# Kernel tuning notes

Measured on AMD Instinct MI355X. Metric: run time of the kernel, lower is better.

The kernel has to match this reference:

```python
import jax, jax.numpy as jnp
import numpy as np

B, S, D, H = 2, 2048, 2048, 16
DH = D // H            # 128 head dim
QP = D // 2            # 1024 compressed q dim
KVP = (2 * D) // 3     # 1365 compressed kv dim
RD = DH // 2           # 64 rope dim
ND = DH // 2           # 64 nope dim
FF = 4 * D
THETA = 10000.0


def _ln(x, w, b, eps=1e-5):
    m = jnp.mean(x, -1, keepdims=True)
    v = jnp.mean((x - m) ** 2, -1, keepdims=True)
    return (x - m) * jax.lax.rsqrt(v + eps) * w + b


def _rotate_half(x):
    x1, x2 = jnp.split(x, 2, axis=-1)
    return jnp.concatenate([-x2, x1], axis=-1)


def setup_inputs() -> dict:
    key = jax.random.key(0)
    ks = jax.random.split(key, 9)
    rn = lambda k, shp, s: (s * jax.random.normal(k, shp)).astype(jnp.float32)
    return {
        'x': jax.random.normal(ks[0], (B, S, D), jnp.float32),
        'attn_norm_w': jnp.ones((D,), jnp.float32), 'attn_norm_b': jnp.zeros((D,), jnp.float32),
        'W_dq': rn(ks[1], (D, QP), 0.01),
        'q_ln_w': jnp.ones((QP,), jnp.float32), 'q_ln_b': jnp.zeros((QP,), jnp.float32),
        'W_uq': rn(ks[2], (QP, D), 0.01),
        'W_dkv': rn(ks[3], (D, KVP + RD), 0.01),
        'kv_ln_w': jnp.ones((KVP,), jnp.float32), 'kv_ln_b': jnp.zeros((KVP,), jnp.float32),
        'W_ukv': rn(ks[4], (KVP, D + H * ND), 0.01),
        'W_o': rn(ks[5], (D, D), 0.01),
        'ff_norm_w': jnp.ones((D,), jnp.float32), 'ff_norm_b': jnp.zeros((D,), jnp.float32),
        'W1': rn(ks[6], (D, FF), 0.02), 'b1': jnp.zeros((FF,), jnp.float32),
        'W2': rn(ks[7], (FF, D), 0.02), 'b2': jnp.zeros((D,), jnp.float32),
    }


def reference(x, attn_norm_w, attn_norm_b, W_dq, q_ln_w, q_ln_b, W_uq, W_dkv,
              kv_ln_w, kv_ln_b, W_ukv, W_o, ff_norm_w, ff_norm_b, W1, b1, W2, b2):
    # ---- pre-LN attention ----
    h = _ln(x, attn_norm_w, attn_norm_b)
    # Q path: down-proj, LN, up-proj
    cq = _ln(h @ W_dq, q_ln_w, q_ln_b)                      # [B,S,QP]
    Q = (cq @ W_uq).reshape(B, S, H, DH).transpose(0, 2, 1, 3)  # [B,H,S,DH]
    Qn, Qr = Q[..., :ND], Q[..., ND:]
    # RoPE tables: emb [S, DH/2]; take first RD/2 freqs, tile -> [1,1,S,RD]
    pos = jnp.arange(S, dtype=jnp.float32)
    freqs = 1.0 / (THETA ** (jnp.arange(0, DH, 2, dtype=jnp.float32) / DH))
    emb = pos[:, None] * freqs[None, :]
    cos = jnp.tile(jnp.cos(emb)[:, :RD // 2], (1, 2))[None, None]
    sin = jnp.tile(jnp.sin(emb)[:, :RD // 2], (1, 2))[None, None]
    Qr = Qr * cos + _rotate_half(Qr) * sin
    # KV path: joint down-proj, split latent / shared rope key
    ckv = h @ W_dkv                                          # [B,S,KVP+RD]
    kv_lora, k_rope = ckv[..., :KVP], ckv[..., KVP:]
    kv_lora = _ln(kv_lora, kv_ln_w, kv_ln_b)
    KV = (kv_lora @ W_ukv).reshape(B, S, H, DH + ND).transpose(0, 2, 1, 3)
    K, V = KV[..., :ND], KV[..., ND:]                        # K [B,H,S,ND], V [B,H,S,DH]
    Kr = k_rope[:, None]                                     # [B,1,S,RD] shared across heads
    Kr = Kr * cos + _rotate_half(Kr) * sin
    Kr = jnp.broadcast_to(Kr, (B, H, S, RD))
    q = jnp.concatenate([Qn, Qr], -1)                        # [B,H,S,DH]
    k = jnp.concatenate([K, Kr], -1)                         # [B,H,S,DH]
    scores = jnp.einsum('bhqd,bhkd->bhqk', q, k) / jnp.sqrt(jnp.float32(DH))
    mask = jnp.tril(jnp.ones((S, S), bool))
    scores = jnp.where(mask, scores, jnp.finfo(scores.dtype).min)
    attn = jax.nn.softmax(scores, axis=-1)
    o = jnp.einsum('bhqk,bhkd->bhqd', attn, V).transpose(0, 2, 1, 3).reshape(B, S, D)
    o = o @ W_o.T
    x = x + o  # dropout is identity at eval
    # ---- pre-LN MLP ----
    r = x
    h = _ln(x, ff_norm_w, ff_norm_b)
    h = jax.nn.gelu(h @ W1 + b1, approximate=False) @ W2 + b2
    return r + h, ckv
```

## Files before the change

### kernel.cpp

```cpp
#include <hip/hip_runtime.h>
#include <hip/hip_bf16.h>
#include <math.h>

#define B_ 2
#define S_ 2048
#define D_ 2048
#define H_ 16
#define DH_ 128
#define QP_ 1024
#define KVP_ 1365
#define RD_ 64
#define ND_ 64
#define FF_ 8192
#define T_ (B_*S_)
#define CKW_ (KVP_+RD_)
#define KVW_ 3072
#define KVP_PAD 1408
#define CKW_PAD 1536

typedef __attribute__((ext_vector_type(8))) short short8;
typedef __attribute__((ext_vector_type(4))) short sh4;
typedef __attribute__((ext_vector_type(4))) float floatx4;

__device__ __forceinline__ void gload_lds16(const __hip_bfloat16* g, __hip_bfloat16* l) {
    __builtin_amdgcn_global_load_lds((const __attribute__((address_space(1))) void*)g,
                                     (__attribute__((address_space(3))) void*)l, 16, 0, 0);
}
__device__ __forceinline__ short f2bs(float f) {
    __hip_bfloat16 h = __float2bfloat16(f);
    return *reinterpret_cast<short*>(&h);
}
__device__ __forceinline__ int sw(int row, int g) { return row * 64 + ((g ^ (row & 7)) << 3); }

__device__ __forceinline__ float fast_gelu(float v) {
    float x = v * 0.70710678118654752f;
    float ax = fabsf(x);
    float t = __builtin_amdgcn_rcpf(1.f + 0.3275911f * ax);
    float y = t * (0.254829592f + t * (-0.284496736f + t * (1.421413741f + t * (-1.453152027f + t * 1.061405429f))));
    float e = __expf(-ax * ax);
    float erfv = 1.f - y * e;
    erfv = copysignf(erfv, x);
    return 0.5f * v * (1.f + erfv);
}

__global__ __launch_bounds__(256) void ln_bf16(const float* __restrict__ in, int in_stride,
                                               const float* __restrict__ w, const float* __restrict__ bb,
                                               __hip_bfloat16* __restrict__ out, int out_stride, int N)
{
    int row = blockIdx.x;
    const float* ip = in + (size_t)row * in_stride;
    __hip_bfloat16* op = out + (size_t)row * out_stride;
    int tid = threadIdx.x;
    __shared__ float s1[256], s2[256];
    float sum = 0.f, sq = 0.f;
    bool vec = (((in_stride | N | out_stride) & 3) == 0);
    if (vec) {
        const float4* ip4 = (const float4*)ip;
        int n4 = N >> 2;
        for (int i = tid; i < n4; i += 256) {
            float4 v = ip4[i];
            sum += v.x + v.y + v.z + v.w;
            sq  += v.x * v.x + v.y * v.y + v.z * v.z + v.w * v.w;
        }
        s1[tid] = sum; s2[tid] = sq; __syncthreads();
        for (int s = 128; s > 0; s >>= 1) {
            if (tid < s) { s1[tid] += s1[tid + s]; s2[tid] += s2[tid + s]; }
            __syncthreads();
        }
        float mean = s1[0] / N;
        float var  = s2[0] / N - mean * mean;
        float rstd = rsqrtf(var + 1e-5f);
        const float4* w4 = (const float4*)w;
        const float4* b4 = (const float4*)bb;
        for (int i = tid; i < n4; i += 256) {
            float4 v = ip4[i], wv = w4[i], bv = b4[i];
            sh4 o;
            o[0] = f2bs((v.x - mean) * rstd * wv.x + bv.x);
            o[1] = f2bs((v.y - mean) * rstd * wv.y + bv.y);
            o[2] = f2bs((v.z - mean) * rstd * wv.z + bv.z);
            o[3] = f2bs((v.w - mean) * rstd * wv.w + bv.w);
            *(sh4*)&op[i * 4] = o;
        }
    } else {
        for (int i = tid; i < N; i += 256) { float v = ip[i]; sum += v; sq += v * v; }
        s1[tid] = sum; s2[tid] = sq; __syncthreads();
        for (int s = 128; s > 0; s >>= 1) {
            if (tid < s) { s1[tid] += s1[tid + s]; s2[tid] += s2[tid + s]; }
            __syncthreads();
        }
        float mean = s1[0] / N;
        float var  = s2[0] / N - mean * mean;
        float rstd = rsqrtf(var + 1e-5f);
        for (int i = tid; i < N; i += 256) {
            float v = ip[i];
            op[i] = __float2bfloat16((v - mean) * rstd * w[i] + bb[i]);
        }
    }
    for (int i = N + tid; i < out_stride; i += 256) op[i] = __float2bfloat16(0.f);
}

__global__ __launch_bounds__(256) void transpose_cvt(const float* __restrict__ W, __hip_bfloat16* __restrict__ Wt,
                                                     int K, int N, int Kp)
{
    __shared__ float t[32][33];
    int k0 = blockIdx.x * 32, n0 = blockIdx.y * 32;
    int tx = threadIdx.x & 31, ty = threadIdx.x >> 5;
    for (int r = ty; r < 32; r += 8) {
        int k = k0 + r, n = n0 + tx;
        t[r][tx] = (k < K && n < N) ? W[(size_t)k * N + n] : 0.f;
    }
    __syncthreads();
    for (int r = ty; r < 32; r += 8) {
        int n = n0 + r, k = k0 + tx;
        Wt[(size_t)n * Kp + k] = __float2bfloat16(t[tx][r]);
    }
}

__global__ __launch_bounds__(256) void cvt_bf16(const float* __restrict__ in, __hip_bfloat16* __restrict__ out, int n)
{
    int i = blockIdx.x * 256 + threadIdx.x;
    if (i < n) out[i] = __float2bfloat16(in[i]);
}

template<int EPI, typename CT>
__global__ __launch_bounds__(256) void gemm_bf16(const __hip_bfloat16* __restrict__ A,
                                                 const __hip_bfloat16* __restrict__ Bt,
                                                 CT* __restrict__ C, int M, int N, int Kp, int ldc,
                                                 const float* __restrict__ bias,
                                                 const float* __restrict__ resid)
{
    __shared__ __hip_bfloat16 As[128 * 64];
    __shared__ __hip_bfloat16 Bs[128 * 64];
    int tid = threadIdx.x;
    int gx = gridDim.x;
    int nwg = gx * gridDim.y;
    int o = blockIdx.y * gx + blockIdx.x;
    int sId = ((nwg & 7) == 0) ? ((o & 7) * (nwg >> 3) + (o >> 3)) : o;
    int bm = (sId / gx) * 128;
    int bn = (sId % gx) * 128;
    int wid = tid >> 6, lane = tid & 63;
    int wm = (wid >> 1) * 64, wn = (wid & 1) * 64;
    int lrow = lane & 15;
    int quad = lane >> 4;

    floatx4 acc[4][4];
    #pragma unroll
    for (int i = 0; i < 4; ++i)
        #pragma unroll
        for (int j = 0; j < 4; ++j)
            acc[i][j] = (floatx4){0.f, 0.f, 0.f, 0.f};

    for (int k0 = 0; k0 < Kp; k0 += 64) {
        #pragma unroll
        for (int it = 0; it < 4; ++it) {
            int chunk = it * 256 + tid;
            int row = chunk >> 3, g = chunk & 7;
            int col = (g ^ (row & 7)) << 3;
            gload_lds16(A + (size_t)(bm + row) * Kp + k0 + col, &As[chunk * 8]);
        }
        #pragma unroll
        for (int it = 0; it < 4; ++it) {
            int chunk = it * 256 + tid;
            int row = chunk >> 3, g = chunk & 7;
            int col = (g ^ (row & 7)) << 3;
            gload_lds16(Bt + (size_t)(bn + row) * Kp + k0 + col, &Bs[chunk * 8]);
        }
        __syncthreads();
        #pragma unroll
        for (int kk = 0; kk < 2; ++kk) {
            short8 a[4], b[4];
            #pragma unroll
            for (int i = 0; i < 4; ++i)
                a[i] = *(const short8*)&As[sw(wm + i * 16 + lrow, kk * 4 + quad)];
            #pragma unroll
            for (int j = 0; j < 4; ++j)
                b[j] = *(const short8*)&Bs[sw(wn + j * 16 + lrow, kk * 4 + quad)];
            #pragma unroll
            for (int i = 0; i < 4; ++i)
                #pragma unroll
                for (int j = 0; j < 4; ++j)
                    acc[i][j] = __builtin_amdgcn_mfma_f32_16x16x32_bf16(a[i], b[j], acc[i][j], 0, 0, 0);
        }
        __syncthreads();
    }

    int cq4 = quad * 4;
    #pragma unroll
    for (int i = 0; i < 4; ++i) {
        #pragma unroll
        for (int j = 0; j < 4; ++j) {
            int col = bn + wn + j * 16 + lrow;
            if (col >= N) continue;
            #pragma unroll
            for (int r = 0; r < 4; ++r) {
                int rowg = bm + wm + i * 16 + cq4 + r;
                float v = acc[i][j][r];
                size_t idx = (size_t)rowg * ldc + col;
                if (EPI == 1) v += resid[idx];
                if (EPI == 2) { v += bias[col]; v = fast_gelu(v); }
                if (EPI == 3) { v += bias[col]; v += ((const float*)C)[idx]; }
                C[idx] = (CT)v;
            }
        }
    }
}

#define BAR8() __builtin_amdgcn_s_barrier()
#define SCB8() __builtin_amdgcn_sched_barrier(0)
#define GATE8(nw) asm volatile("s_waitcnt vmcnt(" #nw ")" ::: "memory")

template<int EPI, typename CT>
__global__ __launch_bounds__(512, 1) void gemm_8ph(const __hip_bfloat16* __restrict__ A,
                                                   const __hip_bfloat16* __restrict__ Bt,
                                                   CT* __restrict__ C, int M, int N, int Kp, int ldc,
                                                   const float* __restrict__ bias,
                                                   const float* __restrict__ resid)
{
    __shared__ __hip_bfloat16 As[2][16384];
    __shared__ __hip_bfloat16 Bs[2][16384];

    int tid = threadIdx.x;
    int wid = tid >> 6, lane = tid & 63;
    int lrow = lane & 15, quad = lane >> 4;
    int awm = (wid >> 2) * 128;
    int bwn = (wid & 3) * 64;

    int gx = gridDim.x;
    int nwg = gx * gridDim.y;
    int o = blockIdx.y * gx + blockIdx.x;
    int q8 = nwg >> 3, r8 = nwg & 7;
    int xcd = o & 7, oi = o >> 3;
    int s = (xcd < r8 ? xcd * (q8 + 1) : r8 * (q8 + 1) + (xcd - r8) * q8) + oi;
    int bm = (s / gx) * 256, bn = (s % gx) * 256;

    const __hip_bfloat16* Abm = A  + (size_t)bm * Kp;
    const __hip_bfloat16* Bbn = Bt + (size_t)bn * Kp;

    int drow = tid >> 3;
    int csw  = ((tid & 7) ^ (drow & 7)) << 3;
    int ldst = tid * 8;

#define STAGE8(srcbase, k0v, dst) do { \
    gload_lds16((srcbase) + (size_t)drow * Kp + (k0v) + csw, (dst) + ldst); \
    gload_lds16((srcbase) + (size_t)(drow + 64) * Kp + (k0v) + csw, (dst) + 4096 + ldst); \
  } while (0)

    int abase = awm + lrow;
    int bbase = bwn + lrow;
    int k0off = ((quad       ^ (lrow & 7)) << 3);
    int k1off = (((4 + quad) ^ (lrow & 7)) << 3);

    short8 af[8][2], bfr[4][2];
    floatx4 acc[8][4];
    #pragma unroll
    for (int m = 0; m < 8; ++m)
        #pragma unroll
        for (int n = 0; n < 4; ++n)
            acc[m][n] = (floatx4){0.f, 0.f, 0.f, 0.f};

#define READ_A8(bufp, mh) do { \
    _Pragma("unroll") \
    for (int m = 0; m < 4; ++m) { \
      const __hip_bfloat16* p_ = (bufp) + (abase + ((mh)*4 + m) * 16) * 64; \
      af[(mh)*4 + m][0] = *(const short8*)(p_ + k0off); \
      af[(mh)*4 + m][1] = *(const short8*)(p_ + k1off); \
    } } while (0)

#define READ_B8(bufp, nh) do { \
    _Pragma("unroll") \
    for (int n = 0; n < 2; ++n) { \
      const __hip_bfloat16* p_ = (bufp) + (bbase + ((nh)*2 + n) * 16) * 64; \
      bfr[(nh)*2 + n][0] = *(const short8*)(p_ + k0off); \
      bfr[(nh)*2 + n][1] = *(const short8*)(p_ + k1off); \
    } } while (0)

#define QMFMA8(mh, nh) do { \
    __builtin_amdgcn_s_setprio(1); \
    _Pragma("unroll") \
    for (int kk = 0; kk < 2; ++kk) \
      _Pragma("unroll") \
      for (int m = 0; m < 4; ++m) \
        _Pragma("unroll") \
        for (int n = 0; n < 2; ++n) \
          acc[(mh)*4 + m][(nh)*2 + n] = __builtin_amdgcn_mfma_f32_16x16x32_bf16( \
              af[(mh)*4 + m][kk], bfr[(nh)*2 + n][kk], acc[(mh)*4 + m][(nh)*2 + n], 0, 0, 0); \
    __builtin_amdgcn_s_setprio(0); \
  } while (0)

    STAGE8(Abm,                   0,  &As[0][0]);
    STAGE8(Abm + (size_t)128*Kp,  0,  &As[0][8192]);
    STAGE8(Bbn,                   0,  &Bs[0][0]);
    STAGE8(Bbn + (size_t)128*Kp,  0,  &Bs[0][8192]);
    STAGE8(Abm,                   64, &As[1][0]);
    STAGE8(Abm + (size_t)128*Kp,  64, &As[1][8192]);
    GATE8(4); SCB8(); BAR8();

    int NT = Kp >> 6;
    #pragma unroll 1
    for (int t = 0; t < NT; t += 2) {
        int kn = (t + 1) << 6;
        int k2 = ((t + 2 < NT) ? t + 2 : NT - 1) << 6;
        int k3 = ((t + 3 < NT) ? t + 3 : NT - 1) << 6;

        STAGE8(Bbn, kn, &Bs[1][0]);
        READ_A8(&As[0][0], 0); READ_B8(&Bs[0][0], 0);
        SCB8(); BAR8();
        QMFMA8(0, 0);
        SCB8(); BAR8();
        STAGE8(Bbn + (size_t)128*Kp, kn, &Bs[1][8192]);
        READ_B8(&Bs[0][0], 1);
        SCB8(); BAR8();
        QMFMA8(0, 1);
        SCB8(); BAR8();
        READ_A8(&As[0][0], 1);
        SCB8(); BAR8();
        QMFMA8(1, 1);
        SCB8(); BAR8();
        STAGE8(Abm, k2, &As[0][0]);
        STAGE8(Abm + (size_t)128*Kp, k2, &As[0][8192]);
        SCB8(); BAR8();
        QMFMA8(1, 0);
        GATE8(4); SCB8(); BAR8();
        STAGE8(Bbn, k2, &Bs[0][0]);
        READ_A8(&As[1][0], 0); READ_B8(&Bs[1][0], 0);
        SCB8(); BAR8();
        QMFMA8(0, 0);
        SCB8(); BAR8();
        STAGE8(Bbn + (size_t)128*Kp, k2, &Bs[0][8192]);
        READ_B8(&Bs[1][0], 1);
        SCB8(); BAR8();
        QMFMA8(0, 1);
        SCB8(); BAR8();
        READ_A8(&As[1][0], 1);
        SCB8(); BAR8();
        QMFMA8(1, 1);
        SCB8(); BAR8();
        STAGE8(Abm, k3, &As[1][0]);
        STAGE8(Abm + (size_t)128*Kp, k3, &As[1][8192]);
        SCB8(); BAR8();
        QMFMA8(1, 0);
        GATE8(4); SCB8(); BAR8();
    }
    asm volatile("s_waitcnt vmcnt(0)" ::: "memory");

    int cq4 = quad * 4;
    #pragma unroll
    for (int m = 0; m < 8; ++m) {
        int rowg = bm + awm + m * 16 + cq4;
        #pragma unroll
        for (int n = 0; n < 4; ++n) {
            int col = bn + bwn + n * 16 + lrow;
            #pragma unroll
            for (int r = 0; r < 4; ++r) {
                float v = acc[m][n][r];
                size_t idx = (size_t)(rowg + r) * ldc + col;
                if (EPI == 1) v += resid[idx];
                if (EPI == 2) { v += bias[col]; v = fast_gelu(v); }
                if (EPI == 3) { v += bias[col]; v += ((const float*)C)[idx]; }
                C[idx] = (CT)v;
            }
        }
    }
#undef STAGE8
#undef READ_A8
#undef READ_B8
#undef QMFMA8
}

__global__ __launch_bounds__(256) void rope_q_kernel(float* __restrict__ Q)
{
    int idx = blockIdx.x * 256 + threadIdx.x;
    int i = idx & 31;
    int h = (idx >> 5) & (H_ - 1);
    int t = idx >> 9;
    float f = expf(-(float)i * (9.210340371976184f / 64.0f));
    float ang = (float)(t & (S_ - 1)) * f;
    float sv, cv; sincosf(ang, &sv, &cv);
    float* p = Q + (size_t)t * D_ + h * DH_ + ND_;
    float u = p[i], v = p[i + 32];
    p[i]      = u * cv - v * sv;
    p[i + 32] = v * cv + u * sv;
}

__global__ __launch_bounds__(256) void rope_kr_bf(const float* __restrict__ ckv, __hip_bfloat16* __restrict__ kr)
{
    int idx = blockIdx.x * 256 + threadIdx.x;
    int i = idx & 31;
    int t = idx >> 5;
    float f = expf(-(float)i * (9.210340371976184f / 64.0f));
    float ang = (float)(t & (S_ - 1)) * f;
    float sv, cv; sincosf(ang, &sv, &cv);
    const float* src = ckv + (size_t)t * CKW_ + KVP_;
    float u = src[i], v = src[i + 32];
    kr[(size_t)t * RD_ + i]      = __float2bfloat16(u * cv - v * sv);
    kr[(size_t)t * RD_ + i + 32] = __float2bfloat16(v * cv + u * sv);
}

__global__ __launch_bounds__(256) void vt_pack(const __hip_bfloat16* __restrict__ kvu,
                                               __hip_bfloat16* __restrict__ Vt)
{
    int bh = blockIdx.y; int b = bh >> 4, h = bh & 15;
    int v = threadIdx.x & 127;
    int tg = blockIdx.x * 2 + (threadIdx.x >> 7);
    int t0 = tg * 8;
    short8 o;
    #pragma unroll
    for (int j = 0; j < 8; ++j) {
        __hip_bfloat16 e = kvu[(size_t)(b * S_ + t0 + j) * KVW_ + h * 192 + 64 + v];
        o[j] = *reinterpret_cast<short*>(&e);
    }
    *(short8*)&Vt[((size_t)bh * 128 + v) * S_ + t0] = o;
}

__global__ __launch_bounds__(256) void attn_mfma(const float* __restrict__ Q,
                                                 const __hip_bfloat16* __restrict__ KVU,
                                                 const __hip_bfloat16* __restrict__ KR,
                                                 const __hip_bfloat16* __restrict__ VT,
                                                 __hip_bfloat16* __restrict__ O)
{
    __shared__ __hip_bfloat16 Kls[64 * 64];
    __shared__ __hip_bfloat16 Krls[64 * 64];
    __shared__ __hip_bfloat16 Vls[128 * 64];
    __shared__ __hip_bfloat16 Pls[4 * 32 * 64];

    int tid = threadIdx.x, wid = tid >> 6, lane = tid & 63;
    int lrow = lane & 15, quad = lane >> 4;
    int kq8 = quad * 8;
    int o = blockIdx.y * 16 + blockIdx.x;
    int sId = (o & 7) * 64 + (o >> 3);
    int qtile = 15 - (sId & 15);
    int bh = sId >> 4;
    int b = bh >> 4, h = bh & 15;
    int q0 = qtile * 128, wq = wid * 32;

    const float scale = 0.08838834764831845f;

    short8 bq[2][2], bqr[2][2];
    #pragma unroll
    for (int n = 0; n < 2; ++n) {
        const float* qrow = Q + (size_t)(b * S_ + q0 + wq + n * 16 + lrow) * D_ + h * DH_;
        #pragma unroll
        for (int s = 0; s < 2; ++s) {
            int base = s * 32 + kq8;
            #pragma unroll
            for (int j = 0; j < 8; ++j) {
                bq[n][s][j]  = f2bs(qrow[base + j] * scale);
                bqr[n][s][j] = f2bs(qrow[64 + base + j] * scale);
            }
        }
    }

    float mstate[2] = {-INFINITY, -INFINITY};
    float lstate[2] = {0.f, 0.f};
    floatx4 acco[8][2];
    #pragma unroll
    for (int vt = 0; vt < 8; ++vt)
        #pragma unroll
        for (int n = 0; n < 2; ++n)
            acco[vt][n] = (floatx4){0.f, 0.f, 0.f, 0.f};

    int nk = qtile * 2 + 2;
    int qmax_w = q0 + wq + 31;

    for (int kt = 0; kt < nk; ++kt) {
        int k0 = kt * 64;
        #pragma unroll
        for (int it = 0; it < 2; ++it) {
            int c = it * 256 + tid;
            int row = c >> 3, g = c & 7;
            int col = ((g ^ (row & 7)) << 3);
            gload_lds16(KVU + (size_t)(b * S_ + k0 + row) * KVW_ + h * 192 + col, &Kls[c * 8]);
            gload_lds16(KR + (size_t)(b * S_ + k0 + row) * RD_ + col, &Krls[c * 8]);
        }
        #pragma unroll
        for (int it = 0; it < 4; ++it) {
            int c = it * 256 + tid;
            int row = c >> 3, g = c & 7;
            int col = ((g ^ (row & 7)) << 3);
            gload_lds16(VT + ((size_t)bh * 128 + row) * S_ + k0 + col, &Vls[c * 8]);
        }
        __syncthreads();

        if (k0 <= qmax_w) {
            floatx4 sacc[4][2];
            #pragma unroll
            for (int m = 0; m < 4; ++m)
                #pragma unroll
                for (int n = 0; n < 2; ++n)
                    sacc[m][n] = (floatx4){0.f, 0.f, 0.f, 0.f};
            #pragma unroll
            for (int m = 0; m < 4; ++m) {
                short8 ak[2], akr[2];
                #pragma unroll
                for (int s = 0; s < 2; ++s) {
                    ak[s]  = *(const short8*)&Kls[sw(m * 16 + lrow, s * 4 + quad)];
                    akr[s] = *(const short8*)&Krls[sw(m * 16 + lrow, s * 4 + quad)];
                }
                #pragma unroll
                for (int n = 0; n < 2; ++n)
                    #pragma unroll
                    for (int s = 0; s < 2; ++s) {
                        sacc[m][n] = __builtin_amdgcn_mfma_f32_16x16x32_bf16(ak[s],  bq[n][s],  sacc[m][n], 0, 0, 0);
                        sacc[m][n] = __builtin_amdgcn_mfma_f32_16x16x32_bf16(akr[s], bqr[n][s], sacc[m][n], 0, 0, 0);
                    }
            }
            #pragma unroll
            for (int n = 0; n < 2; ++n) {
                int qg = q0 + wq + n * 16 + lrow;
                float tmax = -INFINITY;
                #pragma unroll
                for (int m = 0; m < 4; ++m)
                    #pragma unroll
                    for (int r = 0; r < 4; ++r) {
                        int kg = k0 + m * 16 + quad * 4 + r;
                        if (kg > qg) sacc[m][n][r] = -1e30f;
                        tmax = fmaxf(tmax, sacc[m][n][r]);
                    }
                tmax = fmaxf(tmax, __shfl_xor(tmax, 16));
                tmax = fmaxf(tmax, __shfl_xor(tmax, 32));
                float mnew = fmaxf(mstate[n], tmax);
                float alpha = __expf(mstate[n] - mnew);
                mstate[n] = mnew;
                float ps = 0.f;
                #pragma unroll
                for (int m = 0; m < 4; ++m) {
                    sh4 pk;
                    #pragma unroll
                    for (int r = 0; r < 4; ++r) {
                        float p = __expf(sacc[m][n][r] - mnew);
                        ps += p;
                        pk[r] = f2bs(p);
                    }
                    int qloc = n * 16 + lrow;
                    int off = wid * 2048 + qloc * 64 + (((m * 2 + (quad >> 1)) ^ (lrow & 7)) << 3) + ((quad & 1) << 2);
                    *(sh4*)&Pls[off] = pk;
                }
                ps += __shfl_xor(ps, 16);
                ps += __shfl_xor(ps, 32);
                lstate[n] = lstate[n] * alpha + ps;
                #pragma unroll
                for (int vt = 0; vt < 8; ++vt)
                    #pragma unroll
                    for (int r = 0; r < 4; ++r)
                        acco[vt][n][r] *= alpha;
            }
            short8 bp[2][2];
            #pragma unroll
            for (int n = 0; n < 2; ++n)
                #pragma unroll
                for (int s = 0; s < 2; ++s)
                    bp[n][s] = *(const short8*)&Pls[wid * 2048 + sw(n * 16 + lrow, s * 4 + quad)];
            #pragma unroll
            for (int vt = 0; vt < 8; ++vt) {
                short8 av[2];
                #pragma unroll
                for (int s = 0; s < 2; ++s)
                    av[s] = *(const short8*)&Vls[sw(vt * 16 + lrow, s * 4 + quad)];
                #pragma unroll
                for (int n = 0; n < 2; ++n)
                    #pragma unroll
                    for (int s = 0; s < 2; ++s)
                        acco[vt][n] = __builtin_amdgcn_mfma_f32_16x16x32_bf16(av[s], bp[n][s], acco[vt][n], 0, 0, 0);
            }
        }
        __syncthreads();
    }

    #pragma unroll
    for (int n = 0; n < 2; ++n) {
        float inv = 1.0f / lstate[n];
        int tok = b * S_ + q0 + wq + n * 16 + lrow;
        #pragma unroll
        for (int vt = 0; vt < 8; ++vt) {
            sh4 o4;
            #pragma unroll
            for (int r = 0; r < 4; ++r) o4[r] = f2bs(acco[vt][n][r] * inv);
            *(sh4*)&O[(size_t)tok * D_ + h * DH_ + vt * 16 + quad * 4] = o4;
        }
    }
}

extern "C" void kernel_launch(void* const* d_in, const int* in_sizes, int n_in,
                              void* d_out, int out_size, void* d_ws, size_t ws_size,
                              hipStream_t stream)
{
    const float* x     = (const float*)d_in[0];
    const float* anw   = (const float*)d_in[1];
    const float* anb   = (const float*)d_in[2];
    const float* W_dq  = (const float*)d_in[3];
    const float* qlw   = (const float*)d_in[4];
    const float* qlb   = (const float*)d_in[5];
    const float* W_uq  = (const float*)d_in[6];
    const float* W_dkv = (const float*)d_in[7];
    const float* kvlw  = (const float*)d_in[8];
    const float* kvlb  = (const float*)d_in[9];
    const float* W_ukv = (const float*)d_in[10];
    const float* W_o   = (const float*)d_in[11];
    const float* fnw   = (const float*)d_in[12];
    const float* fnb   = (const float*)d_in[13];
    const float* W1    = (const float*)d_in[14];
    const float* b1    = (const float*)d_in[15];
    const float* W2    = (const float*)d_in[16];
    const float* b2    = (const float*)d_in[17];

    float* out0 = (float*)d_out;
    float* ckv  = out0 + (size_t)T_ * D_;

    float* ws = (float*)d_ws;
    float* Q  = ws;
    float* cq = Q + (size_t)T_ * D_;
    __hip_bfloat16* kvu_bf = (__hip_bfloat16*)(cq + (size_t)T_ * QP_);
    __hip_bfloat16* kr_bf  = kvu_bf + (size_t)T_ * KVW_;
    __hip_bfloat16* Vt     = kr_bf + (size_t)T_ * RD_;
    __hip_bfloat16* h_bf   = Vt + (size_t)T_ * D_;
    __hip_bfloat16* cq_bf  = h_bf + (size_t)T_ * D_;
    __hip_bfloat16* kvl_bf = cq_bf + (size_t)T_ * QP_;
    __hip_bfloat16* o_bf   = kvl_bf + (size_t)T_ * KVP_PAD;
    __hip_bfloat16* wdq_t  = o_bf + (size_t)T_ * D_;
    __hip_bfloat16* wuq_t  = wdq_t + (size_t)QP_ * D_;
    __hip_bfloat16* wdkv_t = wuq_t + (size_t)D_ * QP_;
    __hip_bfloat16* wukv_t = wdkv_t + (size_t)CKW_PAD * D_;
    __hip_bfloat16* wo_b   = wukv_t + (size_t)KVW_ * KVP_PAD;
    __hip_bfloat16* w1_t   = wo_b + (size_t)D_ * D_;
    __hip_bfloat16* w2_t   = w1_t + (size_t)FF_ * D_;
    __hip_bfloat16* ff1_bf = (__hip_bfloat16*)ws;

    dim3 blk(256);
    dim3 blk8(512);

    { dim3 g(D_ / 32, QP_ / 32);       transpose_cvt<<<g, blk, 0, stream>>>(W_dq,  wdq_t,  D_, QP_, D_); }
    { dim3 g(QP_ / 32, D_ / 32);       transpose_cvt<<<g, blk, 0, stream>>>(W_uq,  wuq_t,  QP_, D_, QP_); }
    { dim3 g(D_ / 32, CKW_PAD / 32);   transpose_cvt<<<g, blk, 0, stream>>>(W_dkv, wdkv_t, D_, CKW_, D_); }
    { dim3 g(KVP_PAD / 32, KVW_ / 32); transpose_cvt<<<g, blk, 0, stream>>>(W_ukv, wukv_t, KVP_, KVW_, KVP_PAD); }
    { int n = D_ * D_;                 cvt_bf16<<<(n + 255) / 256, blk, 0, stream>>>(W_o, wo_b, n); }
    { dim3 g(D_ / 32, FF_ / 32);       transpose_cvt<<<g, blk, 0, stream>>>(W1, w1_t, D_, FF_, D_); }
    { dim3 g(FF_ / 32, D_ / 32);       transpose_cvt<<<g, blk, 0, stream>>>(W2, w2_t, FF_, D_, FF_); }

    ln_bf16<<<T_, blk, 0, stream>>>(x, D_, anw, anb, h_bf, D_, D_);
    { dim3 g(QP_ / 128, T_ / 128);
      gemm_bf16<0, float><<<g, blk, 0, stream>>>(h_bf, wdq_t, cq, T_, QP_, D_, QP_, nullptr, nullptr); }
    ln_bf16<<<T_, blk, 0, stream>>>(cq, QP_, qlw, qlb, cq_bf, QP_, QP_);
    { dim3 g(D_ / 128, T_ / 128);
      gemm_bf16<0, float><<<g, blk, 0, stream>>>(cq_bf, wuq_t, Q, T_, D_, QP_, D_, nullptr, nullptr); }
    rope_q_kernel<<<(T_ * H_ * 32) / 256, blk, 0, stream>>>(Q);
    { dim3 g(CKW_PAD / 128, T_ / 128);
      gemm_bf16<0, float><<<g, blk, 0, stream>>>(h_bf, wdkv_t, ckv, T_, CKW_, D_, CKW_, nullptr, nullptr); }
    ln_bf16<<<T_, blk, 0, stream>>>(ckv, CKW_, kvlw, kvlb, kvl_bf, KVP_PAD, KVP_);
    { dim3 g(KVW_ / 256, T_ / 256);
      gemm_8ph<0, __hip_bfloat16><<<g, blk8, 0, stream>>>(kvl_bf, wukv_t, kvu_bf, T_, KVW_, KVP_PAD, KVW_, nullptr, nullptr); }
    rope_kr_bf<<<(T_ * 32) / 256, blk, 0, stream>>>(ckv, kr_bf);
    { dim3 g(S_ / 16, B_ * H_);
      vt_pack<<<g, blk, 0, stream>>>(kvu_bf, Vt); }
    { dim3 g(16, B_ * H_);
      attn_mfma<<<g, blk, 0, stream>>>(Q, kvu_bf, kr_bf, Vt, o_bf); }
    { dim3 g(D_ / 128, T_ / 128);
      gemm_bf16<1, float><<<g, blk, 0, stream>>>(o_bf, wo_b, out0, T_, D_, D_, D_, nullptr, x); }
    ln_bf16<<<T_, blk, 0, stream>>>(out0, D_, fnw, fnb, h_bf, D_, D_);
    { dim3 g(FF_ / 256, T_ / 256);
      gemm_8ph<2, __hip_bfloat16><<<g, blk8, 0, stream>>>(h_bf, w1_t, ff1_bf, T_, FF_, D_, FF_, b1, nullptr); }
    { dim3 g(D_ / 128, T_ / 128);
      gemm_bf16<3, float><<<g, blk, 0, stream>>>(ff1_bf, w2_t, out0, T_, D_, FF_, D_, b2, nullptr); }
}
```

Before: 1.070 ms.

## Add 256x128-tile 8-wave pipelined GEMM for N=2048 projections

```diff
diff --git a/kernel.cpp b/kernel.cpp
--- a/kernel.cpp
+++ b/kernel.cpp
@@ -307,34 +307,41 @@
         SCB8(); BAR8();
         QMFMA8(0, 0);
         SCB8(); BAR8();
+
         STAGE8(Bbn + (size_t)128*Kp, kn, &Bs[1][8192]);
         READ_B8(&Bs[0][0], 1);
         SCB8(); BAR8();
         QMFMA8(0, 1);
         SCB8(); BAR8();
+
         READ_A8(&As[0][0], 1);
         SCB8(); BAR8();
         QMFMA8(1, 1);
         SCB8(); BAR8();
+
         STAGE8(Abm, k2, &As[0][0]);
         STAGE8(Abm + (size_t)128*Kp, k2, &As[0][8192]);
         SCB8(); BAR8();
         QMFMA8(1, 0);
         GATE8(4); SCB8(); BAR8();
+
         STAGE8(Bbn, k2, &Bs[0][0]);
         READ_A8(&As[1][0], 0); READ_B8(&Bs[1][0], 0);
         SCB8(); BAR8();
         QMFMA8(0, 0);
         SCB8(); BAR8();
+
         STAGE8(Bbn + (size_t)128*Kp, k2, &Bs[0][8192]);
         READ_B8(&Bs[1][0], 1);
         SCB8(); BAR8();
         QMFMA8(0, 1);
         SCB8(); BAR8();
+
         READ_A8(&As[1][0], 1);
         SCB8(); BAR8();
         QMFMA8(1, 1);
         SCB8(); BAR8();
+
         STAGE8(Abm, k3, &As[1][0]);
         STAGE8(Abm + (size_t)128*Kp, k3, &As[1][8192]);
         SCB8(); BAR8();
@@ -365,6 +372,163 @@
 #undef READ_A8
 #undef READ_B8
 #undef QMFMA8
+}
+
+template<int EPI, typename CT>
+__global__ __launch_bounds__(512, 1) void gemm_8ph_n128(const __hip_bfloat16* __restrict__ A,
+                                                        const __hip_bfloat16* __restrict__ Bt,
+                                                        CT* __restrict__ C, int M, int N, int Kp, int ldc,
+                                                        const float* __restrict__ bias,
+                                                        const float* __restrict__ resid)
+{
+    __shared__ __hip_bfloat16 As[2][16384];
+    __shared__ __hip_bfloat16 Bs[2][8192];
+
+    int tid = threadIdx.x;
+    int wid = tid >> 6, lane = tid & 63;
+    int lrow = lane & 15, quad = lane >> 4;
+    int awm = (wid >> 2) * 128;
+    int bwn = (wid & 3) * 32;
+
+    int gx = gridDim.x;
+    int nwg = gx * gridDim.y;
+    int o = blockIdx.y * gx + blockIdx.x;
+    int q8 = nwg >> 3, r8 = nwg & 7;
+    int xcd = o & 7, oi = o >> 3;
+    int s = (xcd < r8 ? xcd * (q8 + 1) : r8 * (q8 + 1) + (xcd - r8) * q8) + oi;
+    int bm = (s / gx) * 256, bn = (s % gx) * 128;
+
+    const __hip_bfloat16* Abm = A  + (size_t)bm * Kp;
+    const __hip_bfloat16* Bbn = Bt + (size_t)bn * Kp;
+
+    int drow = tid >> 3;
+    int csw  = ((tid & 7) ^ (drow & 7)) << 3;
+    int ldst = tid * 8;
+
+#define STAGE_A(k0v, dst) do { \
+    gload_lds16(Abm + (size_t)drow * Kp + (k0v) + csw,         (dst) + ldst); \
+    gload_lds16(Abm + (size_t)(drow + 64) * Kp + (k0v) + csw,  (dst) + 4096 + ldst); \
+    gload_lds16(Abm + (size_t)(drow + 128) * Kp + (k0v) + csw, (dst) + 8192 + ldst); \
+    gload_lds16(Abm + (size_t)(drow + 192) * Kp + (k0v) + csw, (dst) + 12288 + ldst); \
+  } while (0)
+#define STAGE_B(k0v, dst) do { \
+    gload_lds16(Bbn + (size_t)drow * Kp + (k0v) + csw,        (dst) + ldst); \
+    gload_lds16(Bbn + (size_t)(drow + 64) * Kp + (k0v) + csw, (dst) + 4096 + ldst); \
+  } while (0)
+
+    int abase = awm + lrow;
+    int bbase = bwn + lrow;
+    int k0off = ((quad       ^ (lrow & 7)) << 3);
+    int k1off = (((4 + quad) ^ (lrow & 7)) << 3);
+
+    short8 af[8][2], bfr[2][2];
+    floatx4 acc[8][2];
+    #pragma unroll
+    for (int m = 0; m < 8; ++m)
+        #pragma unroll
+        for (int n = 0; n < 2; ++n)
+            acc[m][n] = (floatx4){0.f, 0.f, 0.f, 0.f};
+
+#define READ_A(bufp, mh) do { \
+    _Pragma("unroll") \
+    for (int m = 0; m < 4; ++m) { \
+      const __hip_bfloat16* p_ = (bufp) + (abase + ((mh)*4 + m) * 16) * 64; \
+      af[(mh)*4 + m][0] = *(const short8*)(p_ + k0off); \
+      af[(mh)*4 + m][1] = *(const short8*)(p_ + k1off); \
+    } } while (0)
+
+#define READ_B(bufp, nh) do { \
+      const __hip_bfloat16* p_ = (bufp) + (bbase + (nh) * 16) * 64; \
+      bfr[nh][0] = *(const short8*)(p_ + k0off); \
+      bfr[nh][1] = *(const short8*)(p_ + k1off); \
+    } while (0)
+
+#define QMFMA(mh, nh) do { \
+    __builtin_amdgcn_s_setprio(1); \
+    _Pragma("unroll") \
+    for (int kk = 0; kk < 2; ++kk) \
+      _Pragma("unroll") \
+      for (int m = 0; m < 4; ++m) \
+        acc[(mh)*4 + m][nh] = __builtin_amdgcn_mfma_f32_16x16x32_bf16( \
+            af[(mh)*4 + m][kk], bfr[nh][kk], acc[(mh)*4 + m][nh], 0, 0, 0); \
+    __builtin_amdgcn_s_setprio(0); \
+  } while (0)
+
+    STAGE_A(0,  &As[0][0]);
+    STAGE_B(0,  &Bs[0][0]);
+    STAGE_A(64, &As[1][0]);
+    GATE8(4); SCB8(); BAR8();
+
+    int NT = Kp >> 6;
+    #pragma unroll 1
+    for (int t = 0; t < NT; t += 2) {
+        int kn = (t + 1) << 6;
+        int k2 = ((t + 2 < NT) ? t + 2 : NT - 1) << 6;
+        int k3 = ((t + 3 < NT) ? t + 3 : NT - 1) << 6;
+
+        STAGE_B(kn, &Bs[1][0]);
+        READ_A(&As[0][0], 0); READ_B(&Bs[0][0], 0);
+        SCB8(); BAR8();
+        QMFMA(0, 0);
+        SCB8(); BAR8();
+        READ_B(&Bs[0][0], 1);
+        SCB8(); BAR8();
+        QMFMA(0, 1);
+        SCB8(); BAR8();
+        READ_A(&As[0][0], 1);
+        SCB8(); BAR8();
+        QMFMA(1, 1);
+        SCB8(); BAR8();
+        STAGE_A(k2, &As[0][0]);
+        SCB8(); BAR8();
+        QMFMA(1, 0);
+        GATE8(4); SCB8(); BAR8();
+        STAGE_B(k2, &Bs[0][0]);
+        READ_A(&As[1][0], 0); READ_B(&Bs[1][0], 0);
+        SCB8(); BAR8();
+        QMFMA(0, 0);
+        SCB8(); BAR8();
+
+        READ_B(&Bs[1][0], 1);
+        SCB8(); BAR8();
+        QMFMA(0, 1);
+        SCB8(); BAR8();
+
+        READ_A(&As[1][0], 1);
+        SCB8(); BAR8();
+        QMFMA(1, 1);
+        SCB8(); BAR8();
+
+        STAGE_A(k3, &As[1][0]);
+        SCB8(); BAR8();
+        QMFMA(1, 0);
+        GATE8(4); SCB8(); BAR8();
+    }
+    asm volatile("s_waitcnt vmcnt(0)" ::: "memory");
+
+    int cq4 = quad * 4;
+    #pragma unroll
+    for (int m = 0; m < 8; ++m) {
+        int rowg = bm + awm + m * 16 + cq4;
+        #pragma unroll
+        for (int n = 0; n < 2; ++n) {
+            int col = bn + bwn + n * 16 + lrow;
+            #pragma unroll
+            for (int r = 0; r < 4; ++r) {
+                float v = acc[m][n][r];
+                size_t idx = (size_t)(rowg + r) * ldc + col;
+                if (EPI == 1) v += resid[idx];
+                if (EPI == 2) { v += bias[col]; v = fast_gelu(v); }
+                if (EPI == 3) { v += bias[col]; v += ((const float*)C)[idx]; }
+                C[idx] = (CT)v;
+            }
+        }
+    }
+#undef STAGE_A
+#undef STAGE_B
+#undef READ_A
+#undef READ_B
+#undef QMFMA
 }
 
 __global__ __launch_bounds__(256) void rope_q_kernel(float* __restrict__ Q)
@@ -640,8 +804,8 @@
     { dim3 g(QP_ / 128, T_ / 128);
       gemm_bf16<0, float><<<g, blk, 0, stream>>>(h_bf, wdq_t, cq, T_, QP_, D_, QP_, nullptr, nullptr); }
     ln_bf16<<<T_, blk, 0, stream>>>(cq, QP_, qlw, qlb, cq_bf, QP_, QP_);
-    { dim3 g(D_ / 128, T_ / 128);
-      gemm_bf16<0, float><<<g, blk, 0, stream>>>(cq_bf, wuq_t, Q, T_, D_, QP_, D_, nullptr, nullptr); }
+    { dim3 g(D_ / 128, T_ / 256);
+      gemm_8ph_n128<0, float><<<g, blk8, 0, stream>>>(cq_bf, wuq_t, Q, T_, D_, QP_, D_, nullptr, nullptr); }
     rope_q_kernel<<<(T_ * H_ * 32) / 256, blk, 0, stream>>>(Q);
     { dim3 g(CKW_PAD / 128, T_ / 128);
       gemm_bf16<0, float><<<g, blk, 0, stream>>>(h_bf, wdkv_t, ckv, T_, CKW_, D_, CKW_, nullptr, nullptr); }
@@ -653,11 +817,11 @@
       vt_pack<<<g, blk, 0, stream>>>(kvu_bf, Vt); }
     { dim3 g(16, B_ * H_);
       attn_mfma<<<g, blk, 0, stream>>>(Q, kvu_bf, kr_bf, Vt, o_bf); }
-    { dim3 g(D_ / 128, T_ / 128);
-      gemm_bf16<1, float><<<g, blk, 0, stream>>>(o_bf, wo_b, out0, T_, D_, D_, D_, nullptr, x); }
+    { dim3 g(D_ / 128, T_ / 256);
+      gemm_8ph_n128<1, float><<<g, blk8, 0, stream>>>(o_bf, wo_b, out0, T_, D_, D_, D_, nullptr, x); }
     ln_bf16<<<T_, blk, 0, stream>>>(out0, D_, fnw, fnb, h_bf, D_, D_);
     { dim3 g(FF_ / 256, T_ / 256);
       gemm_8ph<2, __hip_bfloat16><<<g, blk8, 0, stream>>>(h_bf, w1_t, ff1_bf, T_, FF_, D_, FF_, b1, nullptr); }
-    { dim3 g(D_ / 128, T_ / 128);
-      gemm_bf16<3, float><<<g, blk, 0, stream>>>(ff1_bf, w2_t, out0, T_, D_, FF_, D_, b2, nullptr); }
-}
+    { dim3 g(D_ / 128, T_ / 256);
+      gemm_8ph_n128<3, float><<<g, blk8, 0, stream>>>(ff1_bf, w2_t, out0, T_, D_, FF_, D_, b2, nullptr); }
+}
```

Result: no change. 1.054 ms (-1.5%).

## Replace 8-phase GEMM with triple-buffered 256x128 ping-pong GEMM across projections

Applied to the files above, without the earlier changes.

```diff
diff --git a/kernel.cpp b/kernel.cpp
--- a/kernel.cpp
+++ b/kernel.cpp
@@ -205,25 +205,25 @@
     }
 }
 
-#define BAR8() __builtin_amdgcn_s_barrier()
-#define SCB8() __builtin_amdgcn_sched_barrier(0)
-#define GATE8(nw) asm volatile("s_waitcnt vmcnt(" #nw ")" ::: "memory")
+#define BARP() __builtin_amdgcn_s_barrier()
+#define SCBP() __builtin_amdgcn_sched_barrier(0)
+#define GATEP(nw) asm volatile("s_waitcnt vmcnt(" #nw ")" ::: "memory")
 
 template<int EPI, typename CT>
-__global__ __launch_bounds__(512, 1) void gemm_8ph(const __hip_bfloat16* __restrict__ A,
-                                                   const __hip_bfloat16* __restrict__ Bt,
-                                                   CT* __restrict__ C, int M, int N, int Kp, int ldc,
-                                                   const float* __restrict__ bias,
-                                                   const float* __restrict__ resid)
-{
-    __shared__ __hip_bfloat16 As[2][16384];
-    __shared__ __hip_bfloat16 Bs[2][16384];
+__global__ __launch_bounds__(512, 1) void gemm_pp(const __hip_bfloat16* __restrict__ A,
+                                                  const __hip_bfloat16* __restrict__ Bt,
+                                                  CT* __restrict__ C, int M, int N, int Kp, int ldc,
+                                                  const float* __restrict__ bias,
+                                                  const float* __restrict__ resid)
+{
+    __shared__ __hip_bfloat16 As[3][16384];
+    __shared__ __hip_bfloat16 Bs[3][8192];
 
     int tid = threadIdx.x;
     int wid = tid >> 6, lane = tid & 63;
     int lrow = lane & 15, quad = lane >> 4;
-    int awm = (wid >> 2) * 128;
-    int bwn = (wid & 3) * 64;
+    int awm = (wid >> 1) * 64;
+    int bwn = (wid & 1) * 64;
 
     int gx = gridDim.x;
     int nwg = gx * gridDim.y;
@@ -231,7 +231,7 @@
     int q8 = nwg >> 3, r8 = nwg & 7;
     int xcd = o & 7, oi = o >> 3;
     int s = (xcd < r8 ? xcd * (q8 + 1) : r8 * (q8 + 1) + (xcd - r8) * q8) + oi;
-    int bm = (s / gx) * 256, bn = (s % gx) * 256;
+    int bm = (s / gx) * 256, bn = (s % gx) * 128;
 
     const __hip_bfloat16* Abm = A  + (size_t)bm * Kp;
     const __hip_bfloat16* Bbn = Bt + (size_t)bn * Kp;
@@ -240,112 +240,75 @@
     int csw  = ((tid & 7) ^ (drow & 7)) << 3;
     int ldst = tid * 8;
 
-#define STAGE8(srcbase, k0v, dst) do { \
-    gload_lds16((srcbase) + (size_t)drow * Kp + (k0v) + csw, (dst) + ldst); \
-    gload_lds16((srcbase) + (size_t)(drow + 64) * Kp + (k0v) + csw, (dst) + 4096 + ldst); \
+#define PSTAGE_A(k0v, dst) do { \
+    gload_lds16(Abm + (size_t)drow * Kp + (k0v) + csw,         (dst) + ldst); \
+    gload_lds16(Abm + (size_t)(drow + 64) * Kp + (k0v) + csw,  (dst) + 4096 + ldst); \
+    gload_lds16(Abm + (size_t)(drow + 128) * Kp + (k0v) + csw, (dst) + 8192 + ldst); \
+    gload_lds16(Abm + (size_t)(drow + 192) * Kp + (k0v) + csw, (dst) + 12288 + ldst); \
   } while (0)
-
-    int abase = awm + lrow;
-    int bbase = bwn + lrow;
+#define PSTAGE_B(k0v, dst) do { \
+    gload_lds16(Bbn + (size_t)drow * Kp + (k0v) + csw,        (dst) + ldst); \
+    gload_lds16(Bbn + (size_t)(drow + 64) * Kp + (k0v) + csw, (dst) + 4096 + ldst); \
+  } while (0)
+
     int k0off = ((quad       ^ (lrow & 7)) << 3);
     int k1off = (((4 + quad) ^ (lrow & 7)) << 3);
 
-    short8 af[8][2], bfr[4][2];
-    floatx4 acc[8][4];
-    #pragma unroll
-    for (int m = 0; m < 8; ++m)
+    short8 af0[4], af1[4], bf0[4], bf1[4];
+    floatx4 acc[4][4];
+    #pragma unroll
+    for (int m = 0; m < 4; ++m)
         #pragma unroll
         for (int n = 0; n < 4; ++n)
             acc[m][n] = (floatx4){0.f, 0.f, 0.f, 0.f};
 
-#define READ_A8(bufp, mh) do { \
+#define PREAD(bufA, bufB, dA, dB, koff) do { \
     _Pragma("unroll") \
-    for (int m = 0; m < 4; ++m) { \
-      const __hip_bfloat16* p_ = (bufp) + (abase + ((mh)*4 + m) * 16) * 64; \
-      af[(mh)*4 + m][0] = *(const short8*)(p_ + k0off); \
-      af[(mh)*4 + m][1] = *(const short8*)(p_ + k1off); \
-    } } while (0)
-
-#define READ_B8(bufp, nh) do { \
+    for (int m = 0; m < 4; ++m) \
+      dA[m] = *(const short8*)((bufA) + (awm + m * 16 + lrow) * 64 + (koff)); \
     _Pragma("unroll") \
-    for (int n = 0; n < 2; ++n) { \
-      const __hip_bfloat16* p_ = (bufp) + (bbase + ((nh)*2 + n) * 16) * 64; \
-      bfr[(nh)*2 + n][0] = *(const short8*)(p_ + k0off); \
-      bfr[(nh)*2 + n][1] = *(const short8*)(p_ + k1off); \
-    } } while (0)
-
-#define QMFMA8(mh, nh) do { \
+    for (int n = 0; n < 4; ++n) \
+      dB[n] = *(const short8*)((bufB) + (bwn + n * 16 + lrow) * 64 + (koff)); \
+  } while (0)
+
+#define PMFMA(fa, fb) do { \
     __builtin_amdgcn_s_setprio(1); \
     _Pragma("unroll") \
-    for (int kk = 0; kk < 2; ++kk) \
+    for (int m = 0; m < 4; ++m) \
       _Pragma("unroll") \
-      for (int m = 0; m < 4; ++m) \
-        _Pragma("unroll") \
-        for (int n = 0; n < 2; ++n) \
-          acc[(mh)*4 + m][(nh)*2 + n] = __builtin_amdgcn_mfma_f32_16x16x32_bf16( \
-              af[(mh)*4 + m][kk], bfr[(nh)*2 + n][kk], acc[(mh)*4 + m][(nh)*2 + n], 0, 0, 0); \
+      for (int n = 0; n < 4; ++n) \
+        acc[m][n] = __builtin_amdgcn_mfma_f32_16x16x32_bf16(fa[m], fb[n], acc[m][n], 0, 0, 0); \
     __builtin_amdgcn_s_setprio(0); \
   } while (0)
 
-    STAGE8(Abm,                   0,  &As[0][0]);
-    STAGE8(Abm + (size_t)128*Kp,  0,  &As[0][8192]);
-    STAGE8(Bbn,                   0,  &Bs[0][0]);
-    STAGE8(Bbn + (size_t)128*Kp,  0,  &Bs[0][8192]);
-    STAGE8(Abm,                   64, &As[1][0]);
-    STAGE8(Abm + (size_t)128*Kp,  64, &As[1][8192]);
-    GATE8(4); SCB8(); BAR8();
+    __hip_bfloat16 *aC = &As[0][0], *aN = &As[1][0], *aS = &As[2][0];
+    __hip_bfloat16 *bC = &Bs[0][0], *bN = &Bs[1][0], *bS = &Bs[2][0];
 
     int NT = Kp >> 6;
+
+    PSTAGE_A(0, aC);  PSTAGE_B(0, bC);
+    PSTAGE_A(64, aN); PSTAGE_B(64, bN);
+    GATEP(6); SCBP(); BARP(); SCBP();
+    PREAD(aC, bC, af0, bf0, k0off);
+
     #pragma unroll 1
-    for (int t = 0; t < NT; t += 2) {
-        int kn = (t + 1) << 6;
-        int k2 = ((t + 2 < NT) ? t + 2 : NT - 1) << 6;
-        int k3 = ((t + 3 < NT) ? t + 3 : NT - 1) << 6;
-
-        STAGE8(Bbn, kn, &Bs[1][0]);
-        READ_A8(&As[0][0], 0); READ_B8(&Bs[0][0], 0);
-        SCB8(); BAR8();
-        QMFMA8(0, 0);
-        SCB8(); BAR8();
-        STAGE8(Bbn + (size_t)128*Kp, kn, &Bs[1][8192]);
-        READ_B8(&Bs[0][0], 1);
-        SCB8(); BAR8();
-        QMFMA8(0, 1);
-        SCB8(); BAR8();
-        READ_A8(&As[0][0], 1);
-        SCB8(); BAR8();
-        QMFMA8(1, 1);
-        SCB8(); BAR8();
-        STAGE8(Abm, k2, &As[0][0]);
-        STAGE8(Abm + (size_t)128*Kp, k2, &As[0][8192]);
-        SCB8(); BAR8();
-        QMFMA8(1, 0);
-        GATE8(4); SCB8(); BAR8();
-        STAGE8(Bbn, k2, &Bs[0][0]);
-        READ_A8(&As[1][0], 0); READ_B8(&Bs[1][0], 0);
-        SCB8(); BAR8();
-        QMFMA8(0, 0);
-        SCB8(); BAR8();
-        STAGE8(Bbn + (size_t)128*Kp, k2, &Bs[0][8192]);
-        READ_B8(&Bs[1][0], 1);
-        SCB8(); BAR8();
-        QMFMA8(0, 1);
-        SCB8(); BAR8();
-        READ_A8(&As[1][0], 1);
-        SCB8(); BAR8();
-        QMFMA8(1, 1);
-        SCB8(); BAR8();
-        STAGE8(Abm, k3, &As[1][0]);
-        STAGE8(Abm + (size_t)128*Kp, k3, &As[1][8192]);
-        SCB8(); BAR8();
-        QMFMA8(1, 0);
-        GATE8(4); SCB8(); BAR8();
+    for (int t = 0; t < NT; ++t) {
+        int ks = ((t + 2 < NT) ? t + 2 : NT - 1) << 6;
+        PSTAGE_A(ks, aS); PSTAGE_B(ks, bS);
+        PREAD(aC, bC, af1, bf1, k1off);
+        PMFMA(af0, bf0);
+        GATEP(6); SCBP(); BARP(); SCBP();
+        PREAD(aN, bN, af0, bf0, k0off);
+        PMFMA(af1, bf1);
+        SCBP(); BARP(); SCBP();
+        __hip_bfloat16* ta = aC; aC = aN; aN = aS; aS = ta;
+        __hip_bfloat16* tb = bC; bC = bN; bN = bS; bS = tb;
     }
     asm volatile("s_waitcnt vmcnt(0)" ::: "memory");
 
     int cq4 = quad * 4;
     #pragma unroll
-    for (int m = 0; m < 8; ++m) {
+    for (int m = 0; m < 4; ++m) {
         int rowg = bm + awm + m * 16 + cq4;
         #pragma unroll
         for (int n = 0; n < 4; ++n) {
@@ -361,10 +324,10 @@
             }
         }
     }
-#undef STAGE8
-#undef READ_A8
-#undef READ_B8
-#undef QMFMA8
+#undef PSTAGE_A
+#undef PSTAGE_B
+#undef PREAD
+#undef PMFMA
 }
 
 __global__ __launch_bounds__(256) void rope_q_kernel(float* __restrict__ Q)
@@ -640,24 +603,24 @@
     { dim3 g(QP_ / 128, T_ / 128);
       gemm_bf16<0, float><<<g, blk, 0, stream>>>(h_bf, wdq_t, cq, T_, QP_, D_, QP_, nullptr, nullptr); }
     ln_bf16<<<T_, blk, 0, stream>>>(cq, QP_, qlw, qlb, cq_bf, QP_, QP_);
-    { dim3 g(D_ / 128, T_ / 128);
-      gemm_bf16<0, float><<<g, blk, 0, stream>>>(cq_bf, wuq_t, Q, T_, D_, QP_, D_, nullptr, nullptr); }
+    { dim3 g(D_ / 128, T_ / 256);
+      gemm_pp<0, float><<<g, blk8, 0, stream>>>(cq_bf, wuq_t, Q, T_, D_, QP_, D_, nullptr, nullptr); }
     rope_q_kernel<<<(T_ * H_ * 32) / 256, blk, 0, stream>>>(Q);
     { dim3 g(CKW_PAD / 128, T_ / 128);
       gemm_bf16<0, float><<<g, blk, 0, stream>>>(h_bf, wdkv_t, ckv, T_, CKW_, D_, CKW_, nullptr, nullptr); }
     ln_bf16<<<T_, blk, 0, stream>>>(ckv, CKW_, kvlw, kvlb, kvl_bf, KVP_PAD, KVP_);
-    { dim3 g(KVW_ / 256, T_ / 256);
-      gemm_8ph<0, __hip_bfloat16><<<g, blk8, 0, stream>>>(kvl_bf, wukv_t, kvu_bf, T_, KVW_, KVP_PAD, KVW_, nullptr, nullptr); }
+    { dim3 g(KVW_ / 128, T_ / 256);
+      gemm_pp<0, __hip_bfloat16><<<g, blk8, 0, stream>>>(kvl_bf, wukv_t, kvu_bf, T_, KVW_, KVP_PAD, KVW_, nullptr, nullptr); }
     rope_kr_bf<<<(T_ * 32) / 256, blk, 0, stream>>>(ckv, kr_bf);
     { dim3 g(S_ / 16, B_ * H_);
       vt_pack<<<g, blk, 0, stream>>>(kvu_bf, Vt); }
     { dim3 g(16, B_ * H_);
       attn_mfma<<<g, blk, 0, stream>>>(Q, kvu_bf, kr_bf, Vt, o_bf); }
-    { dim3 g(D_ / 128, T_ / 128);
-      gemm_bf16<1, float><<<g, blk, 0, stream>>>(o_bf, wo_b, out0, T_, D_, D_, D_, nullptr, x); }
+    { dim3 g(D_ / 128, T_ / 256);
+      gemm_pp<1, float><<<g, blk8, 0, stream>>>(o_bf, wo_b, out0, T_, D_, D_, D_, nullptr, x); }
     ln_bf16<<<T_, blk, 0, stream>>>(out0, D_, fnw, fnb, h_bf, D_, D_);
-    { dim3 g(FF_ / 256, T_ / 256);
-      gemm_8ph<2, __hip_bfloat16><<<g, blk8, 0, stream>>>(h_bf, w1_t, ff1_bf, T_, FF_, D_, FF_, b1, nullptr); }
-    { dim3 g(D_ / 128, T_ / 128);
-      gemm_bf16<3, float><<<g, blk, 0, stream>>>(ff1_bf, w2_t, out0, T_, D_, FF_, D_, b2, nullptr); }
-}
+    { dim3 g(FF_ / 128, T_ / 256);
+      gemm_pp<2, __hip_bfloat16><<<g, blk8, 0, stream>>>(h_bf, w1_t, ff1_bf, T_, FF_, D_, FF_, b1, nullptr); }
+    { dim3 g(D_ / 128, T_ / 256);
+      gemm_pp<3, float><<<g, blk8, 0, stream>>>(ff1_bf, w2_t, out0, T_, D_, FF_, D_, b2, nullptr); }
+}
```

Result: faster. 999.1 us (-6.7%).
